# Optimization experiments

Hardware: AMD Instinct MI355X
Metric: run time of the kernel (lower is better)

## Reference

```python
import math
import jax, jax.numpy as jnp
import numpy as np

B, C = 4, 128
H_B, W_B = 512, 512          # BEV size
H_C, W_C = 64, 2048          # cylinder size (z-bins x phi)
MAX_RANGE = 50.0
XMIN, XMAX, YMIN, YMAX = -50.0, 50.0, -50.0, 50.0


def setup_inputs() -> dict:
    key = jax.random.key(0)
    bev_feat = jax.random.normal(key, (B, C, H_B, W_B), dtype=jnp.float32)
    return {"bev_feat": bev_feat}


def reference(bev_feat):
    # Build sampling locations. In the torch module the pixel coords are
    # normalized to [-1,1] and grid_sample(align_corners=True) un-normalizes
    # them back to exactly x_pix / y_pix, so we sample at pixel coords directly.
    phi = jnp.linspace(-math.pi, math.pi, W_C)
    x_g = MAX_RANGE * jnp.cos(phi)
    y_g = MAX_RANGE * jnp.sin(phi)
    x = (x_g - XMIN) / (XMAX - XMIN) * (W_B - 1)   # [W_C] pixel x
    y = (YMAX - y_g) / (YMAX - YMIN) * (H_B - 1)   # [W_C] pixel y

    # Bilinear interpolation with zero padding. The grid is identical for
    # every cylinder row, so sample once per phi column and broadcast.
    x0 = jnp.floor(x).astype(jnp.int32); x1 = x0 + 1
    y0 = jnp.floor(y).astype(jnp.int32); y1 = y0 + 1
    wx1 = x - x0; wx0 = 1.0 - wx1
    wy1 = y - y0; wy0 = 1.0 - wy1

    def corner(xi, yi, w):
        valid = (xi >= 0) & (xi < W_B) & (yi >= 0) & (yi < H_B)
        xi_c = jnp.clip(xi, 0, W_B - 1)
        yi_c = jnp.clip(yi, 0, H_B - 1)
        v = bev_feat[:, :, yi_c, xi_c]            # [B, C, W_C]
        return v * (w * valid)[None, None, :]

    col = (corner(x0, y0, wx0 * wy0) + corner(x1, y0, wx1 * wy0)
           + corner(x0, y1, wx0 * wy1) + corner(x1, y1, wx1 * wy1))
    # broadcast across the H_C z-bins -> [B, C, H_C, W_C]
    return jnp.broadcast_to(col[:, :, None, :], (col.shape[0], col.shape[1], H_C, W_C))
```

## Files before the change

kernel.cpp:

```cpp
#include <hip/hip_runtime.h>
#include <math.h>


namespace {
constexpr int BB = 4, CC = 128, HB = 512, WB = 512, HC = 64, WC = 2048;
constexpr float XMIN = -50.0f, XMAX = 50.0f, YMIN = -50.0f, YMAX = 50.0f;
constexpr float MAX_RANGE = 50.0f;

__device__ __forceinline__ float sample_col(const float* __restrict__ img, int j) {
    const float PI = 3.14159265358979323846f;
    float phi = -PI + (float)j * (2.0f * PI / (float)(WC - 1));
    float xg = MAX_RANGE * cosf(phi);
    float yg = MAX_RANGE * sinf(phi);
    float x = (xg - XMIN) * ((float)(WB - 1) / (XMAX - XMIN));
    float y = (YMAX - yg) * ((float)(HB - 1) / (YMAX - YMIN));
    float fx0 = floorf(x), fy0 = floorf(y);
    int x0 = (int)fx0, y0 = (int)fy0;
    int x1 = x0 + 1, y1 = y0 + 1;
    float wx1 = x - fx0, wx0 = 1.0f - wx1;
    float wy1 = y - fy0, wy0 = 1.0f - wy1;

    float acc = 0.0f;
    {
        bool v = (x0 >= 0) & (x0 < WB) & (y0 >= 0) & (y0 < HB);
        int xc = min(max(x0, 0), WB - 1), yc = min(max(y0, 0), HB - 1);
        acc += img[yc * WB + xc] * (v ? wx0 * wy0 : 0.0f);
    }
    {
        bool v = (x1 >= 0) & (x1 < WB) & (y0 >= 0) & (y0 < HB);
        int xc = min(max(x1, 0), WB - 1), yc = min(max(y0, 0), HB - 1);
        acc += img[yc * WB + xc] * (v ? wx1 * wy0 : 0.0f);
    }
    {
        bool v = (x0 >= 0) & (x0 < WB) & (y1 >= 0) & (y1 < HB);
        int xc = min(max(x0, 0), WB - 1), yc = min(max(y1, 0), HB - 1);
        acc += img[yc * WB + xc] * (v ? wx0 * wy1 : 0.0f);
    }
    {
        bool v = (x1 >= 0) & (x1 < WB) & (y1 >= 0) & (y1 < HB);
        int xc = min(max(x1, 0), WB - 1), yc = min(max(y1, 0), HB - 1);
        acc += img[yc * WB + xc] * (v ? wx1 * wy1 : 0.0f);
    }
    return acc;
}
}

__global__ __launch_bounds__(256) void col_kernel(const float* __restrict__ bev,
                                                  float* __restrict__ col) {
    int t = blockIdx.x * 256 + threadIdx.x;
    int bc = t >> 11;
    int j  = t & (WC - 1);
    const float* img = bev + (size_t)bc * (size_t)(HB * WB);
    col[t] = sample_col(img, j);
}

__global__ __launch_bounds__(256) void bcast_kernel(const float* __restrict__ col,
                                                    float* __restrict__ out) {
    int t = blockIdx.x * 256 + threadIdx.x;
    int bc = t >> 15;
    int r  = t & 32767;
    int jq = r & 511;
    const float4* colv = (const float4*)col;
    float4 v = colv[(bc << 9) + jq];
    ((float4*)out)[t] = v;
}

extern "C" void kernel_launch(void* const* d_in, const int* in_sizes, int n_in,
                              void* d_out, int out_size, void* d_ws, size_t ws_size,
                              hipStream_t stream) {
    const float* bev = (const float*)d_in[0];
    float* out = (float*)d_out;
    float* col = (float*)d_ws;

    col_kernel<<<dim3(BB * CC * WC / 256), dim3(256), 0, stream>>>(bev, col);
    bcast_kernel<<<dim3(BB * CC * HC * WC / 4 / 256), dim3(256), 0, stream>>>(col, out);
}
```

Measured before the change: 662.3 us.

## Fuse column sampling and broadcast into one kernel using shared memory

Merges the bilinear column-sampling kernel and the broadcast kernel into a single kernel with one block per (batch, channel). The sampled column is kept in LDS and then each thread writes its two float4 values across all 64 z-bins. This removes the workspace round trip and a second launch. The trade-off is far fewer blocks (512), which may limit memory-level parallelism on the store stream.

```diff
diff --git a/kernel.cpp b/kernel.cpp
--- a/kernel.cpp
+++ b/kernel.cpp
@@ -45,33 +45,38 @@
 }
 }
 
-__global__ __launch_bounds__(256) void col_kernel(const float* __restrict__ bev,
-                                                  float* __restrict__ col) {
-    int t = blockIdx.x * 256 + threadIdx.x;
-    int bc = t >> 11;
-    int j  = t & (WC - 1);
+__global__ __launch_bounds__(256) void fused_bev2cyl(const float* __restrict__ bev,
+                                                     float* __restrict__ out) {
+    __shared__ __align__(16) float col[WC];
+
+    const int bc  = blockIdx.x;
+    const int tid = threadIdx.x;
     const float* img = bev + (size_t)bc * (size_t)(HB * WB);
-    col[t] = sample_col(img, j);
-}
 
-__global__ __launch_bounds__(256) void bcast_kernel(const float* __restrict__ col,
-                                                    float* __restrict__ out) {
-    int t = blockIdx.x * 256 + threadIdx.x;
-    int bc = t >> 15;
-    int r  = t & 32767;
-    int jq = r & 511;
+    #pragma unroll
+    for (int k = 0; k < WC / 256; ++k) {
+        int j = tid + k * 256;
+        col[j] = sample_col(img, j);
+    }
+    __syncthreads();
+
     const float4* colv = (const float4*)col;
-    float4 v = colv[(bc << 9) + jq];
-    ((float4*)out)[t] = v;
+    float4 va = colv[tid];
+    float4 vb = colv[tid + 256];
+
+    float4* o = (float4*)out + (size_t)bc * (size_t)(HC * WC / 4);
+    #pragma unroll 4
+    for (int h = 0; h < HC; ++h) {
+        o[h * (WC / 4) + tid]       = va;
+        o[h * (WC / 4) + 256 + tid] = vb;
+    }
 }
 
 extern "C" void kernel_launch(void* const* d_in, const int* in_sizes, int n_in,
                               void* d_out, int out_size, void* d_ws, size_t ws_size,
                               hipStream_t stream) {
+    (void)d_ws; (void)ws_size;
     const float* bev = (const float*)d_in[0];
     float* out = (float*)d_out;
-    float* col = (float*)d_ws;
-
-    col_kernel<<<dim3(BB * CC * WC / 256), dim3(256), 0, stream>>>(bev, col);
-    bcast_kernel<<<dim3(BB * CC * HC * WC / 4 / 256), dim3(256), 0, stream>>>(col, out);
+    fused_bev2cyl<<<dim3(BB * CC), dim3(256), 0, stream>>>(bev, out);
 }
```

Measured after the change: 665.7 us. Within noise of the previous version (+0.5%).
